# Optimization experiments

Measured on AMD Instinct MI355X. Metric: run time of the kernel, lower is better.

Reference implementation:

```python
import jax, jax.numpy as jnp
import numpy as np

B = 32          # num graphs
N = 4096        # nodes per graph (temporal length after reshape)
TOT = B * N     # 131072 total nodes
F = 64          # num_features
HS = 128        # hidden_dim_s
RS = 32         # rank_s
HT = 128        # hidden_dim_t
RT = 32         # rank_t
E = 1048576     # num edges


def setup_inputs() -> dict:
    key = jax.random.key(0)
    ks = jax.random.split(key, 20)
    x = jax.random.normal(ks[0], (TOT, F), jnp.float32)
    edge_index = jax.random.randint(ks[1], (2, E), 0, TOT, dtype=jnp.int64)
    batch = jnp.repeat(jnp.arange(B, dtype=jnp.int64), N)

    def lin(k, fan_in, fan_out):
        s = 1.0 / np.sqrt(fan_in)
        return jax.random.uniform(k, (fan_in, fan_out), jnp.float32, -s, s)

    def conv(k, cout, cin):
        s = 1.0 / np.sqrt(cin * 3)
        return jax.random.uniform(k, (cout, cin, 3), jnp.float32, -s, s)

    return {
        "x": x, "edge_index": edge_index, "batch": batch,
        "W1": lin(ks[2], F, HS), "b1": jnp.zeros((HS,), jnp.float32),
        "W2": lin(ks[3], HS, RS), "b2": jnp.zeros((RS,), jnp.float32),
        "W3": lin(ks[4], RS, HS), "b3": jnp.zeros((HS,), jnp.float32),
        "tW1": conv(ks[5], HT, HS), "tb1": jnp.zeros((HT,), jnp.float32),
        "tW2": conv(ks[6], RT, HT), "tb2": jnp.zeros((RT,), jnp.float32),
        "tW3": conv(ks[7], HT, RT), "tb3": jnp.zeros((HT,), jnp.float32),
        "Wpi": lin(ks[8], HT, 1), "bpi": jnp.zeros((1,), jnp.float32),
        "Wn": lin(ks[9], HT, 1), "bn": jnp.zeros((1,), jnp.float32),
        "Wp": lin(ks[10], HT, 1), "bp": jnp.zeros((1,), jnp.float32),
    }


def reference(x, edge_index, batch,
              W1, b1, W2, b2, W3, b3,
              tW1, tb1, tW2, tb2, tW3, tb3,
              Wpi, bpi, Wn, bn, Wp, bp):
    src, dst = edge_index[0], edge_index[1]
    n = x.shape[0]

    # GCN symmetric normalization with added self-loops (PyG GCNConv default)
    deg = jnp.zeros((n,), x.dtype).at[dst].add(1.0) + 1.0  # +1 self-loop
    dinv = jax.lax.rsqrt(deg)
    enorm = dinv[src] * dinv[dst]       # [E] edge normalization
    snorm = dinv * dinv                 # [n] self-loop normalization

    def gcn(h, W, b):
        h = h @ W                                            # [n, out]
        agg = jnp.zeros_like(h).at[dst].add(h[src] * enorm[:, None])
        return agg + h * snorm[:, None] + b

    xs = jax.nn.relu(gcn(x, W1, b1))
    xs = jax.nn.relu(gcn(xs, W2, b2))
    xs = jax.nn.relu(gcn(xs, W3, b3))    # [TOT, HS]

    num_graphs = B  # == batch.max() + 1 (batch is repeat(arange(B), N))
    xs = xs.reshape(num_graphs, -1, xs.shape[-1]).transpose(0, 2, 1)  # [B, HS, N]

    def conv1d(z, w, bias):
        y = jax.lax.conv_general_dilated(
            z, w, window_strides=(1,), padding=((1, 1),),
            dimension_numbers=("NCH", "OIH", "NCH"))
        return y + bias[None, :, None]

    xt = jax.nn.relu(conv1d(xs, tW1, tb1))
    xt = jax.nn.relu(conv1d(xt, tW2, tb2))
    xt = jax.nn.relu(conv1d(xt, tW3, tb3))                   # [B, HT, N]

    xt = xt.transpose(0, 2, 1).reshape(-1, xt.shape[1])      # [TOT, HT]

    pi = jax.nn.sigmoid(xt @ Wpi + bpi)
    nb = jax.nn.softplus(xt @ Wn + bn)
    p = jax.nn.sigmoid(xt @ Wp + bp)
    return (pi, nb, p)
```

## Files before the change

### kernel.cpp

```cpp
#include <hip/hip_runtime.h>
#include <cmath>

constexpr int TOT = 131072;
constexpr int NE  = 1048576;
constexpr int NMASK = 4095;

constexpr int NB   = 512;
constexpr int DPB  = 256;
constexpr int BCAP = 4096;
constexpr int EPB  = 2048;

typedef __attribute__((ext_vector_type(8))) short bf16x8;
typedef __attribute__((ext_vector_type(4))) float f32x4;

__device__ inline float bf2f(unsigned int u16) {
    union { unsigned int i; float f; } x; x.i = u16 << 16; return x.f;
}
__device__ inline unsigned short f2bf(float f) {
    union { float f; unsigned int i; } x; x.f = f;
    unsigned int r = (x.i + 0x7fffu + ((x.i >> 16) & 1u)) >> 16;
    return (unsigned short)r;
}
__device__ inline void unpack8(uint4 v, float* f) {
    f[0] = bf2f(v.x & 0xffffu); f[1] = bf2f(v.x >> 16);
    f[2] = bf2f(v.y & 0xffffu); f[3] = bf2f(v.y >> 16);
    f[4] = bf2f(v.z & 0xffffu); f[5] = bf2f(v.z >> 16);
    f[6] = bf2f(v.w & 0xffffu); f[7] = bf2f(v.w >> 16);
}
__device__ inline uint4 pack8(const float* f) {
    uint4 v;
    v.x = (unsigned)f2bf(f[0]) | ((unsigned)f2bf(f[1]) << 16);
    v.y = (unsigned)f2bf(f[2]) | ((unsigned)f2bf(f[3]) << 16);
    v.z = (unsigned)f2bf(f[4]) | ((unsigned)f2bf(f[5]) << 16);
    v.w = (unsigned)f2bf(f[6]) | ((unsigned)f2bf(f[7]) << 16);
    return v;
}

__device__ inline void pack_one(const float* __restrict__ w, unsigned short* __restrict__ wp,
                                int CIN, int COUT, int taps, int idx) {
    int j = idx & 7;
    int L = (idx >> 3) & 63;
    int f = idx >> 9;
    int NT = COUT >> 4;
    int kc = f / NT, nt = f - kc * NT;
    int k = kc * 32 + (L >> 4) * 8 + j;
    int n = nt * 16 + (L & 15);
    float v;
    if (taps == 1) v = w[k * COUT + n];
    else { int t = k / CIN, c = k - t * CIN; v = w[(n * CIN + c) * 3 + t]; }
    wp[idx] = f2bf(v);
}

struct PackArgs {
    const float *W1, *W2, *W3, *tW1, *tW2, *tW3;
    unsigned short *g1, *g2, *g3, *c1, *c2, *c3;
};
__global__ __launch_bounds__(256) void k_part(const int* __restrict__ src,
                                              const int* __restrict__ dst,
                                              int* __restrict__ gcur,
                                              unsigned* __restrict__ buf,
                                              PackArgs pa) {
    __shared__ int hist[NB];
    __shared__ int cbase[NB];
    __shared__ int lcur[NB];
    const int tid = threadIdx.x;
    const int e0 = blockIdx.x * EPB;

    for (int b = tid; b < NB; b += 256) hist[b] = 0;
    __syncthreads();
    for (int i = tid; i < EPB; i += 256)
        atomicAdd(&hist[dst[e0 + i] >> 8], 1);
    __syncthreads();
    for (int b = tid; b < NB; b += 256) {
        int c = hist[b];
        cbase[b] = (c > 0) ? atomicAdd(&gcur[b * 32], c) : 0;
        lcur[b] = 0;
    }
    __syncthreads();
    for (int i = tid; i < EPB; i += 256) {
        int e = e0 + i;
        int d = dst[e];
        int b = d >> 8;
        int p = atomicAdd(&lcur[b], 1);
        buf[b * BCAP + cbase[b] + p] = ((unsigned)src[e] << 8) | (unsigned)(d & 255);
    }
    int gid = blockIdx.x * 256 + tid;
    if      (gid <  8192) pack_one(pa.W1,  pa.g1, 64, 128, 1, gid);
    else if (gid < 12288) pack_one(pa.W2,  pa.g2, 128, 32, 1, gid - 8192);
    else if (gid < 16384) pack_one(pa.W3,  pa.g3, 32, 128, 1, gid - 12288);
    else if (gid < 65536) pack_one(pa.tW1, pa.c1, 128, 128, 3, gid - 16384);
    else if (gid < 77824) pack_one(pa.tW2, pa.c2, 128, 32, 3, gid - 65536);
    else if (gid < 90112) pack_one(pa.tW3, pa.c3, 32, 128, 3, gid - 77824);
}

__global__ __launch_bounds__(256) void k_bcsr(const unsigned* __restrict__ buf,
                                              const int* __restrict__ gcur,
                                              int* __restrict__ adj,
                                              int2* __restrict__ rse,
                                              float* __restrict__ dinv,
                                              const float4* __restrict__ x,
                                              uint4* __restrict__ xsc) {
    __shared__ int cnt[DPB];
    __shared__ int start[DPB];
    __shared__ int cur[DPB];
    __shared__ int sc[DPB];
    const int b = blockIdx.x;
    const int tid = threadIdx.x;
    cnt[tid] = 0;
    __syncthreads();
    const int n = gcur[b * 32];
    const unsigned* eb = buf + b * BCAP;
    for (int i = tid; i < n; i += 256)
        atomicAdd(&cnt[eb[i] & 255u], 1);
    __syncthreads();
    int v = cnt[tid];
    sc[tid] = v;
    __syncthreads();
    for (int off = 1; off < 256; off <<= 1) {
        int a = sc[tid];
        int p = (tid >= off) ? sc[tid - off] : 0;
        __syncthreads();
        sc[tid] = a + p;
        __syncthreads();
    }
    int st = sc[tid] - v;
    start[tid] = st;
    cur[tid] = 0;
    int d = (b << 8) + tid;
    rse[d] = make_int2(b * BCAP + st, v);
    dinv[d] = rsqrtf((float)v + 1.0f);
    __syncthreads();
    for (int i = tid; i < n; i += 256) {
        unsigned w = eb[i];
        int dl = (int)(w & 255u);
        int p = atomicAdd(&cur[dl], 1);
        adj[b * BCAP + start[dl] + p] = (int)(w >> 8);
    }
    for (int i = tid; i < DPB * 8; i += 256) {
        int rl = i >> 3;
        int t = (b << 11) + i;
        float dv = rsqrtf((float)cnt[rl] + 1.0f);
        float4 v0 = x[t * 2], v1 = x[t * 2 + 1];
        float f[8] = { v0.x * dv, v0.y * dv, v0.z * dv, v0.w * dv,
                       v1.x * dv, v1.y * dv, v1.z * dv, v1.w * dv };
        xsc[t] = pack8(f);
    }
}

template<int LC>
__global__ __launch_bounds__(256) void k_gcsr(const uint4* __restrict__ xs,
                                              const int* __restrict__ adj,
                                              const int2* __restrict__ rse,
                                              const float* __restrict__ dinv,
                                              const float* __restrict__ bias,
                                              uint4* __restrict__ out) {
    int t = blockIdx.x * 256 + threadIdx.x;
    int d = t >> LC;
    int g = t & ((1 << LC) - 1);
    float a[8];
    unpack8(xs[t], a);
    int2 se = rse[d];
    int e = se.x, end = se.x + se.y;
    for (; e + 4 <= end; e += 4) {
        int s0 = adj[e], s1 = adj[e + 1], s2 = adj[e + 2], s3 = adj[e + 3];
        uint4 v0 = xs[(s0 << LC) + g];
        uint4 v1 = xs[(s1 << LC) + g];
        uint4 v2 = xs[(s2 << LC) + g];
        uint4 v3 = xs[(s3 << LC) + g];
        float f[8];
        unpack8(v0, f);
#pragma unroll
        for (int j = 0; j < 8; ++j) a[j] += f[j];
        unpack8(v1, f);
#pragma unroll
        for (int j = 0; j < 8; ++j) a[j] += f[j];
        unpack8(v2, f);
#pragma unroll
        for (int j = 0; j < 8; ++j) a[j] += f[j];
        unpack8(v3, f);
#pragma unroll
        for (int j = 0; j < 8; ++j) a[j] += f[j];
    }
    for (; e < end; ++e) {
        float f[8];
        unpack8(xs[(adj[e] << LC) + g], f);
#pragma unroll
        for (int j = 0; j < 8; ++j) a[j] += f[j];
    }
    float dv = dinv[d];
#pragma unroll
    for (int j = 0; j < 8; ++j)
        a[j] = fmaxf(fmaf(a[j], dv, bias[g * 8 + j]), 0.0f) * dv;
    out[t] = pack8(a);
}

template<int CIN, bool RELU>
__global__ __launch_bounds__(256) void k_gmm(const uint4* __restrict__ xs,
                                             const int* __restrict__ adj,
                                             const int2* __restrict__ rse,
                                             const float* __restrict__ dinv,
                                             const bf16x8* __restrict__ wp,
                                             const float* __restrict__ bias,
                                             unsigned short* __restrict__ y) {
    constexpr int COUT = 128;
    constexpr int ROWS = 64;
    constexpr int SC = CIN + 8;
    constexpr int NV = CIN / 8;
    constexpr int VPT = NV / 4;
    constexpr int NK = CIN / 32;
    constexpr int NT = COUT / 16;
    constexpr int WN = 2, WM = 4;
    __shared__ __attribute__((aligned(16))) unsigned short tile[ROWS * SC];

    const int R0 = blockIdx.x * ROWS;
    const int tid = threadIdx.x;

    {
        int r = R0 + (tid >> 2);
        int g = tid & 3;
        const uint4* base = xs + (long)r * NV + g * VPT;
        float a[VPT * 8];
#pragma unroll
        for (int v = 0; v < VPT; ++v) unpack8(base[v], a + v * 8);
        int2 se = rse[r];
        int e = se.x, end = se.x + se.y;
        for (; e + 4 <= end; e += 4) {
            int s0 = adj[e], s1 = adj[e + 1], s2 = adj[e + 2], s3 = adj[e + 3];
            const uint4* p0 = xs + (long)s0 * NV + g * VPT;
            const uint4* p1 = xs + (long)s1 * NV + g * VPT;
            const uint4* p2 = xs + (long)s2 * NV + g * VPT;
            const uint4* p3 = xs + (long)s3 * NV + g * VPT;
            uint4 v0[VPT], v1[VPT], v2[VPT], v3[VPT];
#pragma unroll
            for (int v = 0; v < VPT; ++v) { v0[v] = p0[v]; v1[v] = p1[v]; v2[v] = p2[v]; v3[v] = p3[v]; }
            float f[VPT * 8];
#pragma unroll
            for (int v = 0; v < VPT; ++v) unpack8(v0[v], f + v * 8);
#pragma unroll
            for (int j = 0; j < VPT * 8; ++j) a[j] += f[j];
#pragma unroll
            for (int v = 0; v < VPT; ++v) unpack8(v1[v], f + v * 8);
#pragma unroll
            for (int j = 0; j < VPT * 8; ++j) a[j] += f[j];
#pragma unroll
            for (int v = 0; v < VPT; ++v) unpack8(v2[v], f + v * 8);
#pragma unroll
            for (int j = 0; j < VPT * 8; ++j) a[j] += f[j];
#pragma unroll
            for (int v = 0; v < VPT; ++v) unpack8(v3[v], f + v * 8);
#pragma unroll
            for (int j = 0; j < VPT * 8; ++j) a[j] += f[j];
        }
        for (; e < end; ++e) {
            const uint4* p0 = xs + (long)adj[e] * NV + g * VPT;
            float f[VPT * 8];
#pragma unroll
            for (int v = 0; v < VPT; ++v) unpack8(p0[v], f + v * 8);
#pragma unroll
            for (int j = 0; j < VPT * 8; ++j) a[j] += f[j];
        }
        float dv = dinv[r];
#pragma unroll
        for (int j = 0; j < VPT * 8; ++j) a[j] *= dv;
        uint4* dst4 = (uint4*)(tile + (tid >> 2) * SC + g * VPT * 8);
#pragma unroll
        for (int v = 0; v < VPT; ++v) dst4[v] = pack8(a + v * 8);
    }
    __syncthreads();

    const int lane = threadIdx.x & 63;
    const int w = threadIdx.x >> 6;
    const int l16 = lane & 15;
    const int q = lane >> 4;
    const int colbase = w * 32;
    const int nt0 = colbase >> 4;

    f32x4 acc[WM][WN];
#pragma unroll
    for (int wm = 0; wm < WM; ++wm)
#pragma unroll
        for (int nt = 0; nt < WN; ++nt) acc[wm][nt] = (f32x4){0.f, 0.f, 0.f, 0.f};

    const bf16x8* __restrict__ wpl = wp + lane;

#pragma unroll
    for (int kc = 0; kc < NK; ++kc) {
        bf16x8 a[WM];
#pragma unroll
        for (int wm = 0; wm < WM; ++wm)
            a[wm] = *(const bf16x8*)(tile + (wm * 16 + l16) * SC + kc * 32 + q * 8);
        bf16x8 b[WN];
#pragma unroll
        for (int nt = 0; nt < WN; ++nt)
            b[nt] = wpl[(kc * NT + nt0 + nt) * 64];
#pragma unroll
        for (int wm = 0; wm < WM; ++wm)
#pragma unroll
            for (int nt = 0; nt < WN; ++nt)
                acc[wm][nt] = __builtin_amdgcn_mfma_f32_16x16x32_bf16(a[wm], b[nt], acc[wm][nt], 0, 0, 0);
    }

#pragma unroll
    for (int wm = 0; wm < WM; ++wm) {
#pragma unroll
        for (int nt = 0; nt < WN; ++nt) {
            int col = colbase + nt * 16 + l16;
            float bi = bias[col];
#pragma unroll
            for (int r = 0; r < 4; ++r) {
                int row = R0 + wm * 16 + q * 4 + r;
                float v = acc[wm][nt][r] + bi;
                if (RELU) v = fmaxf(v, 0.0f);
                y[(long)row * COUT + col] = f2bf(v);
            }
        }
    }
}

template<int CIN, int COUT, int TAPS, bool RELU, bool BIAS, bool SOUT>
__global__ __launch_bounds__(256) void k_mm(const unsigned short* __restrict__ x,
                                            const bf16x8* __restrict__ wp,
                                            const float* __restrict__ bias,
                                            const float* __restrict__ dinv,
                                            unsigned short* __restrict__ y) {
    constexpr int ROWS = 64;
    constexpr int HALO = (TAPS == 3) ? 1 : 0;
    constexpr int TR = ROWS + 2 * HALO;
    constexpr int SC = CIN + 8;
    constexpr int NCH = CIN / 32;
    constexpr int NK = TAPS * NCH;
    constexpr int NT = COUT / 16;
    constexpr int WN = (COUT == 128) ? 2 : 1;
    constexpr int WM = (COUT == 128) ? 4 : 2;
    __shared__ __attribute__((aligned(16))) unsigned short tile[TR * SC];

    const int R0 = blockIdx.x * ROWS;
    const int n0 = R0 & NMASK; (void)n0;

    constexpr int NLD = TR * (CIN / 8);
    for (int idx = threadIdx.x; idx < NLD; idx += 256) {
        int tr = idx / (CIN / 8);
        int c8 = idx - tr * (CIN / 8);
        int ro = tr - HALO;
        bool valid = true;
        if (TAPS == 3) {
            if (ro < 0) valid = (n0 > 0);
            else if (ro >= ROWS) valid = (n0 + ROWS < 4096);
        }
        uint4 v = make_uint4(0, 0, 0, 0);
        if (valid) v = *(const uint4*)(x + (long)(R0 + ro) * CIN + c8 * 8);
        *(uint4*)(tile + tr * SC + c8 * 8) = v;
    }
    __syncthreads();

    const int lane = threadIdx.x & 63;
    const int w = threadIdx.x >> 6;
    const int l16 = lane & 15;
    const int q = lane >> 4;
    const int colbase = (COUT == 128) ? w * 32 : (w & 1) * 16;
    const int rowbase = (COUT == 128) ? 0 : (w >> 1) * 32;
    const int nt0 = colbase >> 4;

    f32x4 acc[WM][WN];
#pragma unroll
    for (int wm = 0; wm < WM; ++wm)
#pragma unroll
        for (int nt = 0; nt < WN; ++nt) acc[wm][nt] = (f32x4){0.f, 0.f, 0.f, 0.f};

    const bf16x8* __restrict__ wpl = wp + lane;

#pragma unroll
    for (int kc = 0; kc < NK; ++kc) {
        const int tap = (TAPS == 3) ? (kc / NCH) : 0;
        const int ch  = (TAPS == 3) ? (kc - tap * NCH) : kc;
        bf16x8 a[WM];
#pragma unroll
        for (int wm = 0; wm < WM; ++wm)
            a[wm] = *(const bf16x8*)(tile + (rowbase + wm * 16 + l16 + tap) * SC + ch * 32 + q * 8);
        bf16x8 b[WN];
#pragma unroll
        for (int nt = 0; nt < WN; ++nt)
            b[nt] = wpl[(kc * NT + nt0 + nt) * 64];
#pragma unroll
        for (int wm = 0; wm < WM; ++wm)
#pragma unroll
            for (int nt = 0; nt < WN; ++nt)
                acc[wm][nt] = __builtin_amdgcn_mfma_f32_16x16x32_bf16(a[wm], b[nt], acc[wm][nt], 0, 0, 0);
    }

#pragma unroll
    for (int wm = 0; wm < WM; ++wm) {
#pragma unroll
        for (int nt = 0; nt < WN; ++nt) {
            int col = colbase + nt * 16 + l16;
            float bi = BIAS ? bias[col] : 0.0f;
#pragma unroll
            for (int r = 0; r < 4; ++r) {
                int row = R0 + rowbase + wm * 16 + q * 4 + r;
                float v = acc[wm][nt][r] + bi;
                if (RELU) v = fmaxf(v, 0.0f);
                if (SOUT) v *= dinv[row];
                y[(long)row * COUT + col] = f2bf(v);
            }
        }
    }
}

__global__ __launch_bounds__(256) void k_c23_heads(
    const unsigned short* __restrict__ x,
    const bf16x8* __restrict__ wp2, const float* __restrict__ tb2,
    const bf16x8* __restrict__ wp3, const float* __restrict__ tb3,
    const float* __restrict__ Wpi, const float* __restrict__ bpi,
    const float* __restrict__ Wn,  const float* __restrict__ bn,
    const float* __restrict__ Wp,  const float* __restrict__ bp,
    float* __restrict__ out) {
    constexpr int SC1 = 136;
    constexpr int SC2 = 40;
    __shared__ __attribute__((aligned(16))) unsigned short shl[82 * 136 + 66 * 40];
    unsigned short* c1  = shl;
    unsigned short* c2  = shl + 82 * 136;
    unsigned short* xts = shl;

    const int R0 = blockIdx.x * 64;
    const int n0 = R0 & NMASK;
    const int tid = threadIdx.x;

    for (int i = tid; i < 82 * 16; i += 256) {
        int r = i >> 4;
        int c8 = i & 15;
        int n = n0 - 2 + r;
        uint4 v = make_uint4(0, 0, 0, 0);
        if (n >= 0 && n < 4096)
            v = *(const uint4*)(x + (long)(R0 - 2 + r) * 128 + c8 * 8);
        *(uint4*)(c1 + r * SC1 + c8 * 8) = v;
    }
    __syncthreads();

    const int lane = tid & 63;
    const int w = tid >> 6;
    const int l16 = lane & 15;
    const int q = lane >> 4;

    for (int rt = w; rt < 5; rt += 4) {
        f32x4 acc[2];
#pragma unroll
        for (int nt = 0; nt < 2; ++nt) acc[nt] = (f32x4){0.f, 0.f, 0.f, 0.f};
        const bf16x8* wpl = wp2 + lane;
#pragma unroll
        for (int kc = 0; kc < 12; ++kc) {
            int tap = kc >> 2, ch = kc & 3;
            bf16x8 a = *(const bf16x8*)(c1 + (16 * rt + l16 + tap) * SC1 + ch * 32 + q * 8);
            bf16x8 b0 = wpl[(kc * 2 + 0) * 64];
            bf16x8 b1 = wpl[(kc * 2 + 1) * 64];
            acc[0] = __builtin_amdgcn_mfma_f32_16x16x32_bf16(a, b0, acc[0], 0, 0, 0);
            acc[1] = __builtin_amdgcn_mfma_f32_16x16x32_bf16(a, b1, acc[1], 0, 0, 0);
        }
#pragma unroll
        for (int nt = 0; nt < 2; ++nt) {
            int col = nt * 16 + l16;
            float bi = tb2[col];
#pragma unroll
            for (int r = 0; r < 4; ++r) {
                int idx = 16 * rt + q * 4 + r;
                if (idx < 66) {
                    int n = n0 - 1 + idx;
                    unsigned short v = 0;
                    if (n >= 0 && n < 4096)
                        v = f2bf(fmaxf(acc[nt][r] + bi, 0.0f));
                    c2[idx * SC2 + col] = v;
                }
            }
        }
    }
    __syncthreads();

    {
        f32x4 acc[4][2];
#pragma unroll
        for (int rt = 0; rt < 4; ++rt)
#pragma unroll
            for (int nt = 0; nt < 2; ++nt) acc[rt][nt] = (f32x4){0.f, 0.f, 0.f, 0.f};
        const bf16x8* wpl = wp3 + lane;
#pragma unroll
        for (int kc = 0; kc < 3; ++kc) {
            bf16x8 a[4];
#pragma unroll
            for (int rt = 0; rt < 4; ++rt)
                a[rt] = *(const bf16x8*)(c2 + (16 * rt + l16 + kc) * SC2 + q * 8);
            bf16x8 b[2];
#pragma unroll
            for (int nt = 0; nt < 2; ++nt)
                b[nt] = wpl[(kc * 8 + 2 * w + nt) * 64];
#pragma unroll
            for (int rt = 0; rt < 4; ++rt)
#pragma unroll
                for (int nt = 0; nt < 2; ++nt)
                    acc[rt][nt] = __builtin_amdgcn_mfma_f32_16x16x32_bf16(a[rt], b[nt], acc[rt][nt], 0, 0, 0);
        }
#pragma unroll
        for (int rt = 0; rt < 4; ++rt) {
#pragma unroll
            for (int nt = 0; nt < 2; ++nt) {
                int col = w * 32 + nt * 16 + l16;
                float bi = tb3[col];
#pragma unroll
                for (int r = 0; r < 4; ++r) {
                    int row = 16 * rt + q * 4 + r;
                    xts[row * 130 + col] = f2bf(fmaxf(acc[rt][nt][r] + bi, 0.0f));
                }
            }
        }
    }
    __syncthreads();

    if (tid < 192) {
        int h = tid >> 6;
        int row = tid & 63;
        const float* Wh = (h == 0) ? Wpi : (h == 1) ? Wn : Wp;
        float s = 0.0f;
        const unsigned short* xr = xts + row * 130;
#pragma unroll
        for (int c2i = 0; c2i < 64; ++c2i) {
            unsigned u = *(const unsigned*)(xr + c2i * 2);
            s = fmaf(bf2f(u & 0xffffu), Wh[c2i * 2], s);
            s = fmaf(bf2f(u >> 16), Wh[c2i * 2 + 1], s);
        }
        float bb = (h == 0) ? bpi[0] : (h == 1) ? bn[0] : bp[0];
        float z = s + bb;
        float o;
        if (h == 1) o = (z > 20.0f) ? z : log1pf(expf(z));
        else        o = 1.0f / (1.0f + expf(-z));
        out[h * TOT + R0 + row] = o;
    }
}

extern "C" void kernel_launch(void* const* d_in, const int* in_sizes, int n_in,
                              void* d_out, int out_size, void* d_ws, size_t ws_size,
                              hipStream_t stream) {
    const float* x   = (const float*)d_in[0];
    const int*   ei  = (const int*)d_in[1];
    const int*   src = ei;
    const int*   dst = ei + NE;
    const float* W1 = (const float*)d_in[3];
    const float* b1 = (const float*)d_in[4];
    const float* W2 = (const float*)d_in[5];
    const float* b2 = (const float*)d_in[6];
    const float* W3 = (const float*)d_in[7];
    const float* b3 = (const float*)d_in[8];
    const float* tW1 = (const float*)d_in[9];
    const float* tb1 = (const float*)d_in[10];
    const float* tW2 = (const float*)d_in[11];
    const float* tb2 = (const float*)d_in[12];
    const float* tW3 = (const float*)d_in[13];
    const float* tb3 = (const float*)d_in[14];
    const float* Wpi = (const float*)d_in[15];
    const float* bpi = (const float*)d_in[16];
    const float* Wn  = (const float*)d_in[17];
    const float* bn  = (const float*)d_in[18];
    const float* Wp  = (const float*)d_in[19];
    const float* bp  = (const float*)d_in[20];

    char* ws = (char*)d_ws;
    float* dinv = (float*)(ws + (0ull << 20));
    int*   gcur = (int*)  (ws + (1ull << 20));
    int2*  rse  = (int2*) (ws + (1ull << 20) + (256 << 10));
    unsigned short* wpG1 = (unsigned short*)(ws + (3ull << 20));
    unsigned short* wpG2 = (unsigned short*)(ws + (3ull << 20) + (128 << 10));
    unsigned short* wpG3 = (unsigned short*)(ws + (3ull << 20) + (256 << 10));
    unsigned short* wpC1 = (unsigned short*)(ws + (3ull << 20) + (384 << 10));
    unsigned short* wpC2 = (unsigned short*)(ws + (3ull << 20) + (512 << 10));
    unsigned short* wpC3 = (unsigned short*)(ws + (3ull << 20) + (640 << 10));
    unsigned* buf = (unsigned*)(ws + (4ull << 20));
    int* adj = (int*)(ws + (12ull << 20));
    unsigned short* Xa = (unsigned short*)(ws + (24ull  << 20));
    unsigned short* Xb = (unsigned short*)(ws + (44ull  << 20));
    unsigned short* Xc = (unsigned short*)(ws + (80ull  << 20));
    unsigned short* Xd = (unsigned short*)(ws + (116ull << 20));
    unsigned short* Xe = (unsigned short*)(ws + (128ull << 20));

    hipMemsetAsync(gcur, 0, NB * 32 * sizeof(int), stream);

    PackArgs pa = { W1, W2, W3, tW1, tW2, tW3, wpG1, wpG2, wpG3, wpC1, wpC2, wpC3 };
    k_part<<<NE / EPB, 256, 0, stream>>>(src, dst, gcur, buf, pa);
    k_bcsr<<<NB, 256, 0, stream>>>(buf, gcur, adj, rse, dinv, (const float4*)x, (uint4*)Xa);

    k_gmm<64, true><<<TOT / 64, 256, 0, stream>>>((const uint4*)Xa, adj, rse, dinv,
                                                  (const bf16x8*)wpG1, b1, Xc);

    k_mm<128, 32, 1, false, false, true>
        <<<TOT / 64, 256, 0, stream>>>(Xc, (const bf16x8*)wpG2, nullptr, dinv, Xd);
    k_gcsr<2><<<TOT * 4 / 256, 256, 0, stream>>>((const uint4*)Xd, adj, rse, dinv,
                                                 b2, (uint4*)Xe);

    k_gmm<32, true><<<TOT / 64, 256, 0, stream>>>((const uint4*)Xe, adj, rse, dinv,
                                                  (const bf16x8*)wpG3, b3, Xb);

    k_mm<128, 128, 3, true, true, false>
        <<<TOT / 64, 256, 0, stream>>>(Xb, (const bf16x8*)wpC1, tb1, nullptr, Xc);

    k_c23_heads<<<TOT / 64, 256, 0, stream>>>(Xc,
                                              (const bf16x8*)wpC2, tb2,
                                              (const bf16x8*)wpC3, tb3,
                                              Wpi, bpi, Wn, bn, Wp, bp, (float*)d_out);
}
```

Before: 287.3 us.

## Fuse first GCN aggregation+GEMM with second-layer projection GEMM

New measurement: 276.7 us. -3.7%, faster.

```diff
diff --git a/kernel.cpp b/kernel.cpp
--- a/kernel.cpp
+++ b/kernel.cpp
@@ -192,6 +192,156 @@
     for (int j = 0; j < 8; ++j)
         a[j] = fmaxf(fmaf(a[j], dv, bias[g * 8 + j]), 0.0f) * dv;
     out[t] = pack8(a);
+}
+
+__global__ __launch_bounds__(256) void k_gmm2(const uint4* __restrict__ xs,
+                                              const int* __restrict__ adj,
+                                              const int2* __restrict__ rse,
+                                              const float* __restrict__ dinv,
+                                              const bf16x8* __restrict__ wp1,
+                                              const float* __restrict__ b1,
+                                              const bf16x8* __restrict__ wp2,
+                                              unsigned short* __restrict__ y) {
+    constexpr int CIN = 64;
+    constexpr int ROWS = 64;
+    constexpr int SC  = CIN + 8;
+    constexpr int SCH = 144;
+    constexpr int NV = CIN / 8;
+    constexpr int VPT = NV / 4;
+    __shared__ __attribute__((aligned(16))) unsigned short tile1[ROWS * SC];
+    __shared__ __attribute__((aligned(16))) unsigned short h1t[ROWS * SCH];
+
+    const int R0 = blockIdx.x * ROWS;
+    const int tid = threadIdx.x;
+
+    {
+        int r = R0 + (tid >> 2);
+        int g = tid & 3;
+        const uint4* base = xs + (long)r * NV + g * VPT;
+        float a[VPT * 8];
+#pragma unroll
+        for (int v = 0; v < VPT; ++v) unpack8(base[v], a + v * 8);
+        int2 se = rse[r];
+        int e = se.x, end = se.x + se.y;
+        for (; e + 4 <= end; e += 4) {
+            int s0 = adj[e], s1 = adj[e + 1], s2 = adj[e + 2], s3 = adj[e + 3];
+            const uint4* p0 = xs + (long)s0 * NV + g * VPT;
+            const uint4* p1 = xs + (long)s1 * NV + g * VPT;
+            const uint4* p2 = xs + (long)s2 * NV + g * VPT;
+            const uint4* p3 = xs + (long)s3 * NV + g * VPT;
+            uint4 v0[VPT], v1[VPT], v2[VPT], v3[VPT];
+#pragma unroll
+            for (int v = 0; v < VPT; ++v) { v0[v] = p0[v]; v1[v] = p1[v]; v2[v] = p2[v]; v3[v] = p3[v]; }
+            float f[VPT * 8];
+#pragma unroll
+            for (int v = 0; v < VPT; ++v) unpack8(v0[v], f + v * 8);
+#pragma unroll
+            for (int j = 0; j < VPT * 8; ++j) a[j] += f[j];
+#pragma unroll
+            for (int v = 0; v < VPT; ++v) unpack8(v1[v], f + v * 8);
+#pragma unroll
+            for (int j = 0; j < VPT * 8; ++j) a[j] += f[j];
+#pragma unroll
+            for (int v = 0; v < VPT; ++v) unpack8(v2[v], f + v * 8);
+#pragma unroll
+            for (int j = 0; j < VPT * 8; ++j) a[j] += f[j];
+#pragma unroll
+            for (int v = 0; v < VPT; ++v) unpack8(v3[v], f + v * 8);
+#pragma unroll
+            for (int j = 0; j < VPT * 8; ++j) a[j] += f[j];
+        }
+        for (; e < end; ++e) {
+            const uint4* p0 = xs + (long)adj[e] * NV + g * VPT;
+            float f[VPT * 8];
+#pragma unroll
+            for (int v = 0; v < VPT; ++v) unpack8(p0[v], f + v * 8);
+#pragma unroll
+            for (int j = 0; j < VPT * 8; ++j) a[j] += f[j];
+        }
+        float dv = dinv[r];
+#pragma unroll
+        for (int j = 0; j < VPT * 8; ++j) a[j] *= dv;
+        uint4* dst4 = (uint4*)(tile1 + (tid >> 2) * SC + g * VPT * 8);
+#pragma unroll
+        for (int v = 0; v < VPT; ++v) dst4[v] = pack8(a + v * 8);
+    }
+    __syncthreads();
+
+    const int lane = tid & 63;
+    const int w = tid >> 6;
+    const int l16 = lane & 15;
+    const int q = lane >> 4;
+
+    {
+        f32x4 acc[4][2];
+#pragma unroll
+        for (int wm = 0; wm < 4; ++wm)
+#pragma unroll
+            for (int nt = 0; nt < 2; ++nt) acc[wm][nt] = (f32x4){0.f, 0.f, 0.f, 0.f};
+        const bf16x8* wpl = wp1 + lane;
+        const int nt0 = w * 2;
+#pragma unroll
+        for (int kc = 0; kc < 2; ++kc) {
+            bf16x8 a[4];
+#pragma unroll
+            for (int wm = 0; wm < 4; ++wm)
+                a[wm] = *(const bf16x8*)(tile1 + (wm * 16 + l16) * SC + kc * 32 + q * 8);
+            bf16x8 b[2];
+#pragma unroll
+            for (int nt = 0; nt < 2; ++nt)
+                b[nt] = wpl[(kc * 8 + nt0 + nt) * 64];
+#pragma unroll
+            for (int wm = 0; wm < 4; ++wm)
+#pragma unroll
+                for (int nt = 0; nt < 2; ++nt)
+                    acc[wm][nt] = __builtin_amdgcn_mfma_f32_16x16x32_bf16(a[wm], b[nt], acc[wm][nt], 0, 0, 0);
+        }
+#pragma unroll
+        for (int wm = 0; wm < 4; ++wm) {
+#pragma unroll
+            for (int nt = 0; nt < 2; ++nt) {
+                int col = w * 32 + nt * 16 + l16;
+                float bi = b1[col];
+#pragma unroll
+                for (int r = 0; r < 4; ++r) {
+                    int row = wm * 16 + q * 4 + r;
+                    h1t[row * SCH + col] = f2bf(fmaxf(acc[wm][nt][r] + bi, 0.0f));
+                }
+            }
+        }
+    }
+    __syncthreads();
+
+    {
+        const int colbase = (w & 1) * 16;
+        const int rowbase = (w >> 1) * 32;
+        const int nt0 = colbase >> 4;
+        f32x4 acc[2];
+#pragma unroll
+        for (int wm = 0; wm < 2; ++wm) acc[wm] = (f32x4){0.f, 0.f, 0.f, 0.f};
+        const bf16x8* wpl = wp2 + lane;
+#pragma unroll
+        for (int kc = 0; kc < 4; ++kc) {
+            bf16x8 a[2];
+#pragma unroll
+            for (int wm = 0; wm < 2; ++wm)
+                a[wm] = *(const bf16x8*)(h1t + (rowbase + wm * 16 + l16) * SCH + kc * 32 + q * 8);
+            bf16x8 b = wpl[(kc * 2 + nt0) * 64];
+#pragma unroll
+            for (int wm = 0; wm < 2; ++wm)
+                acc[wm] = __builtin_amdgcn_mfma_f32_16x16x32_bf16(a[wm], b, acc[wm], 0, 0, 0);
+        }
+#pragma unroll
+        for (int wm = 0; wm < 2; ++wm) {
+            int col = colbase + l16;
+#pragma unroll
+            for (int r = 0; r < 4; ++r) {
+                int row = R0 + rowbase + wm * 16 + q * 4 + r;
+                float v = acc[wm][r] * dinv[row];
+                y[(long)row * 32 + col] = f2bf(v);
+            }
+        }
+    }
 }
 
 template<int CIN, bool RELU>
@@ -584,11 +734,9 @@
     k_part<<<NE / EPB, 256, 0, stream>>>(src, dst, gcur, buf, pa);
     k_bcsr<<<NB, 256, 0, stream>>>(buf, gcur, adj, rse, dinv, (const float4*)x, (uint4*)Xa);
 
-    k_gmm<64, true><<<TOT / 64, 256, 0, stream>>>((const uint4*)Xa, adj, rse, dinv,
-                                                  (const bf16x8*)wpG1, b1, Xc);
-
-    k_mm<128, 32, 1, false, false, true>
-        <<<TOT / 64, 256, 0, stream>>>(Xc, (const bf16x8*)wpG2, nullptr, dinv, Xd);
+    k_gmm2<<<TOT / 64, 256, 0, stream>>>((const uint4*)Xa, adj, rse, dinv,
+                                         (const bf16x8*)wpG1, b1, (const bf16x8*)wpG2, Xd);
+
     k_gcsr<2><<<TOT * 4 / 256, 256, 0, stream>>>((const uint4*)Xd, adj, rse, dinv,
                                                  b2, (uint4*)Xe);
 
```
